# Optimization experiments

Hardware: AMD Instinct MI355X
Metric: run time of the kernel (lower is better)

The kernel has to match this reference:

```python
import jax, jax.numpy as jnp
import numpy as np

EPS = 1e-20


def setup_inputs() -> dict:
    B, N, V = 64, 8, 128000
    key = jax.random.key(0)
    k1, k2, k3 = jax.random.split(key, 3)
    draft_token_ids = jax.random.randint(k1, (B, N), 0, V, dtype=jnp.int64 if jax.config.jax_enable_x64 else jnp.int32)
    # proper probability distributions via softmax over random logits
    draft_probs = jax.nn.softmax(jax.random.normal(k2, (B, N, V), dtype=jnp.float32), axis=-1)
    verify_probs = jax.nn.softmax(jax.random.normal(k3, (B, N + 1, V), dtype=jnp.float32), axis=-1)
    return {
        "draft_token_ids": draft_token_ids,
        "draft_probs": draft_probs,
        "verify_probs": verify_probs,
    }


def reference(draft_token_ids, draft_probs, verify_probs):
    """Chain speculative (rejection) sampling, flashinfer-style.

    Returns:
      output_token_ids:  (B, N+1) int, rejected tail padded with -1
      accepted_token_num:(B,) independent per-token acceptance count
      emitted_token_num: (B,) accepted draft tokens before first rejection
    """
    B, N, V = draft_probs.shape
    key = jax.random.key(1)
    ku, kr, kb = jax.random.split(key, 3)

    tgt = verify_probs[:, :N, :]  # target probs aligned with draft positions
    # gather p = target prob of drafted token, q = draft prob of drafted token
    tok = draft_token_ids[..., None]
    p = jnp.take_along_axis(tgt, tok, axis=2)[..., 0]          # (B, N)
    q = jnp.take_along_axis(draft_probs, tok, axis=2)[..., 0]  # (B, N)

    u = jax.random.uniform(ku, (B, N), dtype=jnp.float32)
    accept = u * q < p                                          # (B, N) bool

    # independent-acceptance metric (alignment of draft vs target)
    accepted_token_num = accept.sum(axis=1).astype(jnp.int32)
    # chain: stop at first rejection
    prefix = jnp.cumprod(accept.astype(jnp.int32), axis=1)      # (B, N)
    emitted_token_num = prefix.sum(axis=1).astype(jnp.int32)    # (B,)

    # recovered distribution at each position: normalize relu(target - draft)
    residual = jnp.maximum(tgt - draft_probs, 0.0)
    residual = residual / jnp.maximum(residual.sum(axis=-1, keepdims=True), EPS)
    recovered = jax.random.categorical(kr, jnp.log(residual + EPS), axis=-1)  # (B, N)

    # bonus token from the extra target distribution (all drafts accepted)
    bonus = jax.random.categorical(kb, jnp.log(verify_probs[:, N, :] + EPS), axis=-1)  # (B,)

    batch_idx = jnp.arange(B)
    rec_at_stop = recovered[batch_idx, jnp.minimum(emitted_token_num, N - 1)]
    final_tok = jnp.where(emitted_token_num < N, rec_at_stop, bonus)  # (B,)

    pos = jnp.arange(N + 1)[None, :]                      # (1, N+1)
    em = emitted_token_num[:, None]                       # (B, 1)
    draft_ext = jnp.concatenate([draft_token_ids, jnp.zeros((B, 1), draft_token_ids.dtype)], axis=1)
    out = jnp.where(pos < em, draft_ext,
                    jnp.where(pos == em, final_tok[:, None].astype(draft_ext.dtype), -1))
    return out, accepted_token_num, emitted_token_num
```

## Files before the change

kernel.cpp:

```cpp
#include <hip/hip_runtime.h>
#include <stdint.h>

constexpr int Bn = 64;
constexpr int Nn = 8;
constexpr int Vn = 128000;
constexpr int CH = 32;
constexpr int CHUNK = Vn / CH;
constexpr int F4 = CHUNK / 4;
constexpr float EPSf = 1e-20f;
constexpr float TINYf = 1.17549435082228751e-38f;

struct TFOut { uint32_t a, b; };

__host__ __device__ constexpr TFOut tf2x32(uint32_t k0, uint32_t k1,
                                           uint32_t x0, uint32_t x1) {
  uint32_t k2 = k0 ^ k1 ^ 0x1BD11BDAu;
  x0 += k0; x1 += k1;
#define TFR(r) { x0 += x1; x1 = (uint32_t)((x1 << (r)) | (x1 >> (32 - (r)))); x1 ^= x0; }
  TFR(13) TFR(15) TFR(26) TFR(6)
  x0 += k1; x1 += k2 + 1u;
  TFR(17) TFR(29) TFR(16) TFR(24)
  x0 += k2; x1 += k0 + 2u;
  TFR(13) TFR(15) TFR(26) TFR(6)
  x0 += k0; x1 += k1 + 3u;
  TFR(17) TFR(29) TFR(16) TFR(24)
  x0 += k1; x1 += k2 + 4u;
  TFR(13) TFR(15) TFR(26) TFR(6)
  x0 += k2; x1 += k0 + 5u;
#undef TFR
  return TFOut{x0, x1};
}

constexpr TFOut KU = tf2x32(0u, 1u, 0u, 0u);
constexpr TFOut KR = tf2x32(0u, 1u, 0u, 1u);
constexpr TFOut KB_ = tf2x32(0u, 1u, 0u, 2u);

__device__ __forceinline__ float jax_u01(uint32_t bits) {
  return __uint_as_float((bits >> 9) | 0x3f800000u) - 1.0f;
}

__device__ __forceinline__ uint32_t rbits(uint32_t k0, uint32_t k1, uint32_t t) {
  TFOut o = tf2x32(k0, k1, 0u, t);
  return o.a ^ o.b;
}

__device__ __forceinline__ float gumbel_at(uint32_t k0, uint32_t k1, uint32_t t) {
  float u = jax_u01(rbits(k0, k1, t));
  float uu = fmaxf(TINYf, u + TINYf);
  return -logf(-logf(uu));
}

__device__ __forceinline__ unsigned long long packsc(float s, uint32_t v) {
  uint32_t u = __float_as_uint(s);
  uint32_t m = (u & 0x80000000u) ? ~u : (u | 0x80000000u);
  return ((unsigned long long)m << 32) | (unsigned long long)(~v);
}

__device__ __forceinline__ int accept_bit(int j, const int* __restrict__ ids,
                                          const float* __restrict__ draft,
                                          const float* __restrict__ verify) {
  int b = j >> 3, n = j & 7;
  float u = jax_u01(rbits(KU.a, KU.b, (uint32_t)j));
  int tok = ids[j];
  float p = verify[(size_t)(b * (Nn + 1) + n) * Vn + tok];
  float q = draft[(size_t)(b * Nn + n) * Vn + tok];
  return (u * q < p) ? 1 : 0;
}

__global__ void __launch_bounds__(256)
KA(const int* __restrict__ ids, const float* __restrict__ draft,
   const float* __restrict__ verify, int* __restrict__ out,
   float* __restrict__ partial, unsigned long long* __restrict__ R) {
  int blk = blockIdx.x;
  int b = blk >> 5, c = blk & 31;
  __shared__ int s_acc[8];
  __shared__ float sred[256];
  if (threadIdx.x < 8) s_acc[threadIdx.x] = accept_bit(b * 8 + threadIdx.x, ids, draft, verify);
  __syncthreads();
  int em = 0;
  while (em < 8 && s_acc[em]) em++;

  if (c == 0 && threadIdx.x == 0) {
    int acc = s_acc[0] + s_acc[1] + s_acc[2] + s_acc[3] + s_acc[4] + s_acc[5] + s_acc[6] + s_acc[7];
    out[Bn * (Nn + 1) + b] = acc;
    out[Bn * (Nn + 1) + Bn + b] = em;
    for (int pos = 0; pos <= Nn; pos++)
      out[b * (Nn + 1) + pos] = (pos < em) ? ids[b * Nn + pos] : -1;
    R[b] = 0ull;
  }
  if (em >= Nn) return;

  const float4* t4 = (const float4*)(verify + (size_t)(b * (Nn + 1) + em) * Vn + c * CHUNK);
  const float4* d4 = (const float4*)(draft + (size_t)(b * Nn + em) * Vn + c * CHUNK);
  float s = 0.0f;
  for (int i = threadIdx.x; i < F4; i += 256) {
    float4 t = t4[i], d = d4[i];
    s += fmaxf(t.x - d.x, 0.0f);
    s += fmaxf(t.y - d.y, 0.0f);
    s += fmaxf(t.z - d.z, 0.0f);
    s += fmaxf(t.w - d.w, 0.0f);
  }
  sred[threadIdx.x] = s;
  __syncthreads();
  for (int st = 128; st > 0; st >>= 1) {
    if (threadIdx.x < st) sred[threadIdx.x] += sred[threadIdx.x + st];
    __syncthreads();
  }
  if (threadIdx.x == 0) partial[blk] = sred[0];
}

__global__ void __launch_bounds__(256)
KB(const int* __restrict__ ids, const float* __restrict__ draft,
   const float* __restrict__ verify, const float* __restrict__ partial,
   unsigned long long* __restrict__ R) {
  int blk = blockIdx.x;
  int b = blk >> 5, c = blk & 31;
  __shared__ int s_acc[8];
  __shared__ unsigned long long smax[256];
  if (threadIdx.x < 8) s_acc[threadIdx.x] = accept_bit(b * 8 + threadIdx.x, ids, draft, verify);
  __syncthreads();
  int em = 0;
  while (em < 8 && s_acc[em]) em++;

  float best = -__builtin_inff();
  uint32_t bestv = 0u;

  if (em < Nn) {
    float S = 0.0f;
    for (int i = 0; i < CH; i++) S += partial[b * CH + i];
    float Sm = fmaxf(S, EPSf);
    const float4* t4 = (const float4*)(verify + (size_t)(b * (Nn + 1) + em) * Vn + c * CHUNK);
    const float4* d4 = (const float4*)(draft + (size_t)(b * Nn + em) * Vn + c * CHUNK);
    uint32_t trow = (uint32_t)(b * Nn + em) * (uint32_t)Vn;
    for (int i = threadIdx.x; i < F4; i += 256) {
      float4 t = t4[i], d = d4[i];
      uint32_t v0 = (uint32_t)(c * CHUNK + i * 4);
      float tv[4] = {t.x, t.y, t.z, t.w};
      float dv[4] = {d.x, d.y, d.z, d.w};
#pragma unroll
      for (int k = 0; k < 4; k++) {
        float r = fmaxf(tv[k] - dv[k], 0.0f);
        float logit = logf(r / Sm + EPSf);
        float sc = gumbel_at(KR.a, KR.b, trow + v0 + k) + logit;
        if (sc > best) { best = sc; bestv = v0 + k; }
      }
    }
  } else {
    const float4* p4 = (const float4*)(verify + (size_t)(b * (Nn + 1) + Nn) * Vn + c * CHUNK);
    uint32_t trow = (uint32_t)b * (uint32_t)Vn;
    for (int i = threadIdx.x; i < F4; i += 256) {
      float4 p = p4[i];
      uint32_t v0 = (uint32_t)(c * CHUNK + i * 4);
      float pv[4] = {p.x, p.y, p.z, p.w};
#pragma unroll
      for (int k = 0; k < 4; k++) {
        float logit = logf(pv[k] + EPSf);
        float sc = gumbel_at(KB_.a, KB_.b, trow + v0 + k) + logit;
        if (sc > best) { best = sc; bestv = v0 + k; }
      }
    }
  }

  smax[threadIdx.x] = packsc(best, bestv);
  __syncthreads();
  for (int st = 128; st > 0; st >>= 1) {
    if (threadIdx.x < st) {
      unsigned long long o = smax[threadIdx.x + st];
      if (o > smax[threadIdx.x]) smax[threadIdx.x] = o;
    }
    __syncthreads();
  }
  if (threadIdx.x == 0) atomicMax(&R[b], smax[0]);
}

__global__ void __launch_bounds__(512)
KC(const int* __restrict__ ids, const float* __restrict__ draft,
   const float* __restrict__ verify, const unsigned long long* __restrict__ R,
   int* __restrict__ out) {
  __shared__ int s_acc[512];
  int j = threadIdx.x;
  s_acc[j] = accept_bit(j, ids, draft, verify);
  __syncthreads();
  if (j < Bn) {
    int em = 0;
    while (em < 8 && s_acc[j * 8 + em]) em++;
    int tok = (int)(~(uint32_t)(R[j] & 0xFFFFFFFFull));
    out[j * (Nn + 1) + em] = tok;
  }
}

extern "C" void kernel_launch(void* const* d_in, const int* in_sizes, int n_in,
                              void* d_out, int out_size, void* d_ws, size_t ws_size,
                              hipStream_t stream) {
  const int* ids = (const int*)d_in[0];
  const float* draft = (const float*)d_in[1];
  const float* verify = (const float*)d_in[2];
  int* out = (int*)d_out;

  char* w = (char*)d_ws;
  float* partial = (float*)w;
  unsigned long long* R = (unsigned long long*)(w + 8192);

  KA<<<dim3(Bn * CH), dim3(256), 0, stream>>>(ids, draft, verify, out, partial, R);
  KB<<<dim3(Bn * CH), dim3(256), 0, stream>>>(ids, draft, verify, partial, R);
  KC<<<dim3(1), dim3(512), 0, stream>>>(ids, draft, verify, R, out);
}
```

Measured before the change: 469.7 us.

## Drop final kernel by last-block finalize and pass accept count via workspace

The third kernel is removed. The last block of each batch row, found with an atomic done counter after a threadfence, now writes the sampled token. KB reads the emitted count that KA stored in the workspace instead of recomputing the acceptance bits, and it sums the partials with wavefront shuffles. The aim is to cut one launch and the repeated gathers, at the cost of an extra atomic plus fence per block.

```diff
diff --git a/kernel.cpp b/kernel.cpp
--- a/kernel.cpp
+++ b/kernel.cpp
@@ -31,8 +31,8 @@
   return TFOut{x0, x1};
 }
 
-constexpr TFOut KU = tf2x32(0u, 1u, 0u, 0u);
-constexpr TFOut KR = tf2x32(0u, 1u, 0u, 1u);
+constexpr TFOut KU  = tf2x32(0u, 1u, 0u, 0u);
+constexpr TFOut KR  = tf2x32(0u, 1u, 0u, 1u);
 constexpr TFOut KB_ = tf2x32(0u, 1u, 0u, 2u);
 
 __device__ __forceinline__ float jax_u01(uint32_t bits) {
@@ -70,7 +70,8 @@
 __global__ void __launch_bounds__(256)
 KA(const int* __restrict__ ids, const float* __restrict__ draft,
    const float* __restrict__ verify, int* __restrict__ out,
-   float* __restrict__ partial, unsigned long long* __restrict__ R) {
+   float* __restrict__ partial, unsigned long long* __restrict__ R,
+   int* __restrict__ em_g, int* __restrict__ done) {
   int blk = blockIdx.x;
   int b = blk >> 5, c = blk & 31;
   __shared__ int s_acc[8];
@@ -80,13 +81,18 @@
   int em = 0;
   while (em < 8 && s_acc[em]) em++;
 
-  if (c == 0 && threadIdx.x == 0) {
-    int acc = s_acc[0] + s_acc[1] + s_acc[2] + s_acc[3] + s_acc[4] + s_acc[5] + s_acc[6] + s_acc[7];
-    out[Bn * (Nn + 1) + b] = acc;
-    out[Bn * (Nn + 1) + Bn + b] = em;
-    for (int pos = 0; pos <= Nn; pos++)
-      out[b * (Nn + 1) + pos] = (pos < em) ? ids[b * Nn + pos] : -1;
-    R[b] = 0ull;
+  if (c == 0) {
+    if (threadIdx.x < Nn + 1)
+      out[b * (Nn + 1) + threadIdx.x] =
+          (threadIdx.x < em) ? ids[b * Nn + threadIdx.x] : -1;
+    if (threadIdx.x == 0) {
+      int acc = s_acc[0] + s_acc[1] + s_acc[2] + s_acc[3] + s_acc[4] + s_acc[5] + s_acc[6] + s_acc[7];
+      out[Bn * (Nn + 1) + b] = acc;
+      out[Bn * (Nn + 1) + Bn + b] = em;
+      em_g[b] = em;
+      R[b] = 0ull;
+      done[b] = 0;
+    }
   }
   if (em >= Nn) return;
 
@@ -112,23 +118,23 @@
 __global__ void __launch_bounds__(256)
 KB(const int* __restrict__ ids, const float* __restrict__ draft,
    const float* __restrict__ verify, const float* __restrict__ partial,
-   unsigned long long* __restrict__ R) {
+   unsigned long long* __restrict__ R, const int* __restrict__ em_g,
+   int* __restrict__ done, int* __restrict__ out) {
   int blk = blockIdx.x;
   int b = blk >> 5, c = blk & 31;
-  __shared__ int s_acc[8];
   __shared__ unsigned long long smax[256];
-  if (threadIdx.x < 8) s_acc[threadIdx.x] = accept_bit(b * 8 + threadIdx.x, ids, draft, verify);
-  __syncthreads();
-  int em = 0;
-  while (em < 8 && s_acc[em]) em++;
+  int em = em_g[b];
 
   float best = -__builtin_inff();
   uint32_t bestv = 0u;
 
   if (em < Nn) {
+    float pv = partial[b * CH + (threadIdx.x & 31)];
     float S = 0.0f;
-    for (int i = 0; i < CH; i++) S += partial[b * CH + i];
+#pragma unroll
+    for (int i = 0; i < CH; i++) S += __shfl(pv, i, 64);
     float Sm = fmaxf(S, EPSf);
+
     const float4* t4 = (const float4*)(verify + (size_t)(b * (Nn + 1) + em) * Vn + c * CHUNK);
     const float4* d4 = (const float4*)(draft + (size_t)(b * Nn + em) * Vn + c * CHUNK);
     uint32_t trow = (uint32_t)(b * Nn + em) * (uint32_t)Vn;
@@ -151,10 +157,10 @@
     for (int i = threadIdx.x; i < F4; i += 256) {
       float4 p = p4[i];
       uint32_t v0 = (uint32_t)(c * CHUNK + i * 4);
-      float pv[4] = {p.x, p.y, p.z, p.w};
+      float pvv[4] = {p.x, p.y, p.z, p.w};
 #pragma unroll
       for (int k = 0; k < 4; k++) {
-        float logit = logf(pv[k] + EPSf);
+        float logit = logf(pvv[k] + EPSf);
         float sc = gumbel_at(KB_.a, KB_.b, trow + v0 + k) + logit;
         if (sc > best) { best = sc; bestv = v0 + k; }
       }
@@ -170,22 +176,13 @@
     }
     __syncthreads();
   }
-  if (threadIdx.x == 0) atomicMax(&R[b], smax[0]);
-}
-
-__global__ void __launch_bounds__(512)
-KC(const int* __restrict__ ids, const float* __restrict__ draft,
-   const float* __restrict__ verify, const unsigned long long* __restrict__ R,
-   int* __restrict__ out) {
-  __shared__ int s_acc[512];
-  int j = threadIdx.x;
-  s_acc[j] = accept_bit(j, ids, draft, verify);
-  __syncthreads();
-  if (j < Bn) {
-    int em = 0;
-    while (em < 8 && s_acc[j * 8 + em]) em++;
-    int tok = (int)(~(uint32_t)(R[j] & 0xFFFFFFFFull));
-    out[j * (Nn + 1) + em] = tok;
+  if (threadIdx.x == 0) {
+    atomicMax(&R[b], smax[0]);
+    __threadfence();
+    if (atomicAdd(&done[b], 1) == CH - 1) {
+      unsigned long long rv = atomicAdd(&R[b], 0ull);
+      out[b * (Nn + 1) + em] = (int)(~(uint32_t)(rv & 0xFFFFFFFFull));
+    }
   }
 }
 
@@ -200,8 +197,9 @@
   char* w = (char*)d_ws;
   float* partial = (float*)w;
   unsigned long long* R = (unsigned long long*)(w + 8192);
-
-  KA<<<dim3(Bn * CH), dim3(256), 0, stream>>>(ids, draft, verify, out, partial, R);
-  KB<<<dim3(Bn * CH), dim3(256), 0, stream>>>(ids, draft, verify, partial, R);
-  KC<<<dim3(1), dim3(512), 0, stream>>>(ids, draft, verify, R, out);
-}
+  int* em_g = (int*)(w + 8704);
+  int* done = (int*)(w + 8960);
+
+  KA<<<dim3(Bn * CH), dim3(256), 0, stream>>>(ids, draft, verify, out, partial, R, em_g, done);
+  KB<<<dim3(Bn * CH), dim3(256), 0, stream>>>(ids, draft, verify, partial, R, em_g, done, out);
+}
```

Result: slower. 503.4 us (+7.2%).
